# Kernel optimization log

Measured on AMD Instinct MI355X. Metric: run time of the kernel, lower is better.

The kernel has to match this reference:

```python
import jax, jax.numpy as jnp
import numpy as np

B, S, D, H = 4, 2048, 1024, 16
HD = D // H


def setup_inputs() -> dict:
    key = jax.random.key(0)
    ks = jax.random.split(key, 9)
    s = 1.0 / np.sqrt(D)
    return {
        "x": jax.random.normal(ks[0], (B, S, D), dtype=jnp.float32),
        "wq": jax.random.uniform(ks[1], (D, D), jnp.float32, -s, s),
        "bq": jax.random.uniform(ks[2], (D,), jnp.float32, -s, s),
        "wk": jax.random.uniform(ks[3], (D, D), jnp.float32, -s, s),
        "bk": jax.random.uniform(ks[4], (D,), jnp.float32, -s, s),
        "wv": jax.random.uniform(ks[5], (D, D), jnp.float32, -s, s),
        "bv": jax.random.uniform(ks[6], (D,), jnp.float32, -s, s),
        "wo": jax.random.uniform(ks[7], (D, D), jnp.float32, -s, s),
        "bo": jax.random.uniform(ks[8], (D,), jnp.float32, -s, s),
    }


def reference(x, wq, bq, wk, bk, wv, bv, wo, bo):
    b, s, _ = x.shape
    # QKV projections, split into heads: [B, H, S, HD]
    q = (x @ wq + bq).reshape(b, s, H, HD).transpose(0, 2, 1, 3)
    k = (x @ wk + bk).reshape(b, s, H, HD).transpose(0, 2, 1, 3)
    v = (x @ wv + bv).reshape(b, s, H, HD).transpose(0, 2, 1, 3)
    # Full score matrix [B, H, S, S] as the original does
    scores = jnp.einsum("bhqd,bhkd->bhqk", q, k) / jnp.sqrt(jnp.float32(HD))
    attn = jax.nn.softmax(scores, axis=-1)  # dropout is identity in eval mode
    ctx = jnp.einsum("bhqk,bhkd->bhqd", attn, v)
    ctx = ctx.transpose(0, 2, 1, 3).reshape(b, s, D)
    return ctx @ wo + bo
```

## Files before the change

kernel.cpp:

```cpp
#include <hip/hip_runtime.h>
#include <hip/hip_bf16.h>
#include <stdint.h>

#define B_  4
#define S_  2048
#define D_  1024
#define H_  16
#define HD_ 64

using bf16x8 = __attribute__((ext_vector_type(8))) short;
using f32x2  = __attribute__((ext_vector_type(2))) float;
using f32x4  = __attribute__((ext_vector_type(4))) float;
using f32x8  = __attribute__((ext_vector_type(8))) float;
using f32x16 = __attribute__((ext_vector_type(16))) float;
using i32x2  = __attribute__((ext_vector_type(2))) int;
using i32x4  = __attribute__((ext_vector_type(4))) int;

#define QSCALE 0.18033688011112042f

#if __has_builtin(__builtin_amdgcn_exp2f)
#define EXP2F(x) __builtin_amdgcn_exp2f(x)
#else
#define EXP2F(x) exp2f(x)
#endif

__device__ __forceinline__ short f2b(float f) {
  union { __hip_bfloat16 h; short s; } u;
  u.h = __float2bfloat16(f);
  return u.s;
}

__device__ __forceinline__ unsigned cvtpk(float lo, float hi) {
  unsigned r;
  asm("v_cvt_pk_bf16_f32 %0, %1, %2" : "=v"(r) : "v"(lo), "v"(hi));
  return r;
}

__device__ __forceinline__ void g2lds16(const void* g, void* l) {
  __builtin_amdgcn_global_load_lds(
      (const __attribute__((address_space(1))) uint32_t*)(uintptr_t)g,
      (__attribute__((address_space(3))) uint32_t*)(uint32_t)(uintptr_t)l,
      16, 0, 0);
}


__global__ __launch_bounds__(256) void k_cvt_x(
    const float* __restrict__ x, short* __restrict__ xb, int n8,
    const float* __restrict__ bq, const float* __restrict__ bk,
    const float* __restrict__ bv, float* __restrict__ biasqkv) {
  if (blockIdx.x == gridDim.x - 1) {
#pragma unroll
    for (int j = 0; j < 12; ++j) {
      int i = j * 256 + threadIdx.x;
      float v = (i < D_) ? bq[i] * QSCALE : (i < 2 * D_) ? bk[i - D_] : bv[i - 2 * D_];
      biasqkv[i] = v;
    }
    return;
  }
  int i = blockIdx.x * 256 + threadIdx.x;
  if (i >= n8) return;
  const float4* xp = (const float4*)x;
  float4 a = xp[2 * i], b = xp[2 * i + 1];
  bf16x8 o;
  o[0] = f2b(a.x); o[1] = f2b(a.y); o[2] = f2b(a.z); o[3] = f2b(a.w);
  o[4] = f2b(b.x); o[5] = f2b(b.y); o[6] = f2b(b.z); o[7] = f2b(b.w);
  ((bf16x8*)xb)[i] = o;
}

__global__ __launch_bounds__(256) void k_cvt_w(
    const float* __restrict__ wq, const float* __restrict__ wk,
    const float* __restrict__ wv, const float* __restrict__ wo,
    short* __restrict__ wqkvT, short* __restrict__ woT) {
  __shared__ float tile[32][33];
  int wi = blockIdx.z;
  const float* src = wi == 0 ? wq : wi == 1 ? wk : wi == 2 ? wv : wo;
  float scale = (wi == 0) ? QSCALE : 1.0f;
  short* dst = wi < 3 ? wqkvT + (size_t)wi * D_ * D_ : woT;
  int n0 = blockIdx.x * 32, k0 = blockIdx.y * 32;
  int tx = threadIdx.x, ty = threadIdx.y;
#pragma unroll
  for (int j = 0; j < 4; ++j)
    tile[ty + j * 8][tx] = src[(size_t)(k0 + ty + j * 8) * D_ + n0 + tx];
  __syncthreads();
#pragma unroll
  for (int j = 0; j < 4; ++j)
    dst[(size_t)(n0 + ty + j * 8) * D_ + k0 + tx] = f2b(tile[tx][ty + j * 8] * scale);
}


template <int MODE>
__global__ __launch_bounds__(256, 2) void k_gemm(
    const short* __restrict__ A, const short* __restrict__ Bt,
    const float* __restrict__ bias, float* __restrict__ outF,
    short* __restrict__ Qo, short* __restrict__ Ko, short* __restrict__ Vo) {
  constexpr int K = 1024;
  __shared__ short Als[128 * 64];
  __shared__ short Bls[128 * 64];
  const int tid = threadIdx.x;
  const int wave = tid >> 6, lane = tid & 63;
  const int wr = wave >> 1, wc = wave & 1;
  const int l15 = lane & 15, l4 = lane >> 4;
  const int rowBase = blockIdx.x * 128;
  const int colBase = blockIdx.y * 128;

  f32x4 zero4 = {0.f, 0.f, 0.f, 0.f};
  f32x4 acc[4][4];
#pragma unroll
  for (int m = 0; m < 4; ++m)
#pragma unroll
    for (int n = 0; n < 4; ++n) acc[m][n] = zero4;

  for (int kt = 0; kt < K; kt += 64) {
#pragma unroll
    for (int i = 0; i < 4; ++i) {
      int c = i * 256 + tid;
      int r = c >> 3;
      int ko = ((c & 7) * 8) ^ ((r & 7) << 3);
      g2lds16(A + (size_t)(rowBase + r) * K + kt + ko, &Als[(i * 256 + wave * 64) * 8]);
      g2lds16(Bt + (size_t)(colBase + r) * K + kt + ko, &Bls[(i * 256 + wave * 64) * 8]);
    }
    __syncthreads();
#pragma unroll
    for (int kk = 0; kk < 2; ++kk) {
      bf16x8 af[4], bfr[4];
#pragma unroll
      for (int m = 0; m < 4; ++m) {
        int r = wr * 64 + m * 16 + l15;
        af[m] = *(const bf16x8*)&Als[r * 64 + ((kk * 32 + l4 * 8) ^ ((r & 7) << 3))];
      }
#pragma unroll
      for (int n = 0; n < 4; ++n) {
        int r = wc * 64 + n * 16 + l15;
        bfr[n] = *(const bf16x8*)&Bls[r * 64 + ((kk * 32 + l4 * 8) ^ ((r & 7) << 3))];
      }
#pragma unroll
      for (int m = 0; m < 4; ++m)
#pragma unroll
        for (int n = 0; n < 4; ++n)
          acc[m][n] = __builtin_amdgcn_mfma_f32_16x16x32_bf16(af[m], bfr[n], acc[m][n], 0, 0, 0);
    }
    __syncthreads();
  }

#pragma unroll
  for (int n = 0; n < 4; ++n) {
    int n_g = colBase + wc * 64 + n * 16 + l15;
    float bia = bias[n_g];
#pragma unroll
    for (int m = 0; m < 4; ++m) {
#pragma unroll
      for (int r = 0; r < 4; ++r) {
        int m_g = rowBase + wr * 64 + m * 16 + l4 * 4 + r;
        float v = acc[m][n][r] + bia;
        if constexpr (MODE == 0) {
          int p = n_g >> 10, dm = n_g & 1023, h = dm >> 6, hd = dm & 63;
          int b = m_g >> 11, s = m_g & 2047;
          short* dst = p == 0 ? Qo : p == 1 ? Ko : Vo;
          size_t idx;
          if (p == 2) idx = ((size_t)((b * H_ + h) * HD_ + hd)) * S_ + s;
          else        idx = ((size_t)((b * H_ + h) * S_ + s)) * HD_ + hd;
          dst[idx] = f2b(v);
        } else {
          outF[(size_t)m_g * D_ + n_g] = v;
        }
      }
    }
  }
}


__global__ __launch_bounds__(256, 4) void k_attn2(
    const short* __restrict__ Q, const short* __restrict__ K,
    const short* __restrict__ Vt, short* __restrict__ ctx) {
  const int l = blockIdx.x + (blockIdx.y << 4);
  const int c = l & 7, k = l >> 3;
  const int bh = c + ((k & 7) << 3);
  const int q0 = (k >> 3) * 128;
  const int tid = threadIdx.x, wave = tid >> 6, lane = tid & 63;
  const int l31 = lane & 31, hi = lane >> 5;
  const short* Qb = Q + (size_t)bh * S_ * HD_;
  const short* Kb = K + (size_t)bh * S_ * HD_;
  const short* Vb = Vt + (size_t)bh * HD_ * S_;

  __shared__ short Kls[2][64 * 64];
  __shared__ short Vls[2][64 * 64];

  bf16x8 qf[4];
#pragma unroll
  for (int ks = 0; ks < 4; ++ks)
    qf[ks] = *(const bf16x8*)&Qb[(size_t)(q0 + wave * 32 + l31) * HD_ + ks * 16 + hi * 8];

  bf16x8 ones;
#pragma unroll
  for (int i = 0; i < 8; ++i) ones[i] = (short)0x3F80;

  f32x16 ctxa[2], lacc;
#pragma unroll
  for (int i = 0; i < 16; ++i) { ctxa[0][i] = 0.f; ctxa[1][i] = 0.f; lacc[i] = 0.f; }

#define STAGE(kv0, b)                                                          \
  {                                                                            \
    _Pragma("unroll") for (int i = 0; i < 2; ++i) {                            \
      int cc = i * 256 + tid;                                                  \
      int r = cc >> 3;                                                         \
      int off = ((cc & 7) * 8) ^ ((r & 7) << 3);                               \
      g2lds16(Kb + (size_t)((kv0) + r) * HD_ + off,                            \
              &Kls[b][(i * 256 + wave * 64) * 8]);                             \
      g2lds16(Vb + (size_t)r * S_ + (kv0) + off,                               \
              &Vls[b][(i * 256 + wave * 64) * 8]);                             \
    }                                                                          \
  }

  STAGE(0, 0);
  int buf = 0;
#pragma unroll 1
  for (int t = 0; t < S_ / 64; ++t) {
    __syncthreads();
    STAGE((((t + 1) & 31) * 64), (buf ^ 1));

    f32x16 sa[2];
    __builtin_amdgcn_s_setprio(1);
#pragma unroll
    for (int tt = 0; tt < 2; ++tt) {
#pragma unroll
      for (int i = 0; i < 16; ++i) sa[tt][i] = 0.f;
#pragma unroll
      for (int ks = 0; ks < 4; ++ks) {
        int r = tt * 32 + l31;
        bf16x8 kf = *(const bf16x8*)&Kls[buf][r * 64 + ((ks * 16 + hi * 8) ^ ((r & 7) << 3))];
        sa[tt] = __builtin_amdgcn_mfma_f32_32x32x16_bf16(kf, qf[ks], sa[tt], 0, 0, 0);
      }
    }
    __builtin_amdgcn_s_setprio(0);

#pragma unroll
    for (int tt = 0; tt < 2; ++tt)
#pragma unroll
      for (int i = 0; i < 16; ++i) sa[tt][i] = EXP2F(sa[tt][i]);

    __builtin_amdgcn_s_setprio(1);
#pragma unroll
    for (int ks = 0; ks < 4; ++ks) {
      int tt = ks >> 1, s1 = ks & 1;
      unsigned x0 = cvtpk(sa[tt][8 * s1 + 0], sa[tt][8 * s1 + 1]);
      unsigned x1 = cvtpk(sa[tt][8 * s1 + 2], sa[tt][8 * s1 + 3]);
      unsigned y0 = cvtpk(sa[tt][8 * s1 + 4], sa[tt][8 * s1 + 5]);
      unsigned y1 = cvtpk(sa[tt][8 * s1 + 6], sa[tt][8 * s1 + 7]);
      i32x2 r0 = __builtin_amdgcn_permlane32_swap((int)x0, (int)y0, false, false);
      i32x2 r1 = __builtin_amdgcn_permlane32_swap((int)x1, (int)y1, false, false);
      union { i32x4 i; bf16x8 h; } pu;
      pu.i = (i32x4){r0[0], r1[0], r0[1], r1[1]};
      lacc = __builtin_amdgcn_mfma_f32_32x32x16_bf16(ones, pu.h, lacc, 0, 0, 0);
#pragma unroll
      for (int nn = 0; nn < 2; ++nn) {
        int r = nn * 32 + l31;
        bf16x8 vf = *(const bf16x8*)&Vls[buf][r * 64 + ((ks * 16 + hi * 8) ^ ((r & 7) << 3))];
        ctxa[nn] = __builtin_amdgcn_mfma_f32_32x32x16_bf16(vf, pu.h, ctxa[nn], 0, 0, 0);
      }
    }
    __builtin_amdgcn_s_setprio(0);
    buf ^= 1;
  }

  __syncthreads();
  short* Pw = &Kls[0][0] + wave * 2048;
  float inv = 1.0f / lacc[0];
#pragma unroll
  for (int tt = 0; tt < 2; ++tt)
#pragma unroll
    for (int g = 0; g < 4; ++g) {
      unsigned d0 = cvtpk(ctxa[tt][4 * g + 0] * inv, ctxa[tt][4 * g + 1] * inv);
      unsigned d1 = cvtpk(ctxa[tt][4 * g + 2] * inv, ctxa[tt][4 * g + 3] * inv);
      int hd0 = tt * 32 + g * 8 + hi * 4;
      *(i32x2*)((char*)Pw + l31 * 128 + ((hd0 * 2) ^ ((l31 & 7) << 3))) =
          (i32x2){(int)d0, (int)d1};
    }
  __syncthreads();
  const int b = bh >> 4, h = bh & 15;
#pragma unroll
  for (int p = 0; p < 8; ++p) {
    int cc = p * 64 + lane;
    int q = cc >> 4, s8 = cc & 15;
    i32x2 v = *(const i32x2*)((const char*)Pw + q * 128 + ((s8 * 8) ^ ((q & 7) << 3)));
    int row = q0 + wave * 32 + q;
    *(i32x2*)&ctx[((size_t)(b * S_ + row)) * D_ + h * HD_ + s8 * 4] = v;
  }
}


extern "C" void kernel_launch(void* const* d_in, const int* in_sizes, int n_in,
                              void* d_out, int out_size, void* d_ws, size_t ws_size,
                              hipStream_t stream) {
  const float* x  = (const float*)d_in[0];
  const float* wq = (const float*)d_in[1];
  const float* bq = (const float*)d_in[2];
  const float* wk = (const float*)d_in[3];
  const float* bk = (const float*)d_in[4];
  const float* wv = (const float*)d_in[5];
  const float* bv = (const float*)d_in[6];
  const float* wo = (const float*)d_in[7];
  const float* bo = (const float*)d_in[8];
  float* out = (float*)d_out;

  char* ws = (char*)d_ws;
  short* xb    = (short*)(ws);
  short* wqkvT = (short*)(ws + (16 << 20));
  short* woT   = (short*)(ws + (22 << 20));
  float* biasq = (float*)(ws + (24 << 20));
  short* Qb    = (short*)(ws + (25 << 20));
  short* Kb    = (short*)(ws + (41 << 20));
  short* Vb    = (short*)(ws + (57 << 20));

  k_cvt_x<<<dim3(4097), dim3(256), 0, stream>>>(x, xb, (B_ * S_ * D_) / 8,
                                                bq, bk, bv, biasq);
  k_cvt_w<<<dim3(32, 32, 4), dim3(32, 8), 0, stream>>>(wq, wk, wv, wo, wqkvT, woT);

  k_gemm<0><<<dim3(64, 24), dim3(256), 0, stream>>>(xb, wqkvT, biasq,
                                                    (float*)nullptr, Qb, Kb, Vb);
  k_attn2<<<dim3(S_ / 128, B_ * H_), dim3(256), 0, stream>>>(Qb, Kb, Vb, xb );
  k_gemm<1><<<dim3(64, 8), dim3(256), 0, stream>>>(xb, woT, bo, out,
                                                   nullptr, nullptr, nullptr);
}
```

Before: 183.9 us.

## Software-pipeline QK^T one tile ahead of softmax-PV and replace ones-MFMA row sum

Restructures the attention inner loop so the QK^T MFMAs for the next KV tile are issued while the exp and PV work for the current tile runs, with K and V staged on separate schedules in double-buffered LDS. The row-sum MFMA against a ones vector is replaced by a register reduction plus a cross-half lane shuffle. The GEMM launch bound is raised to ask for three blocks per CU. Holding two sets of score accumulators raises register pressure, and the extra occupancy hint may cause spills in the GEMM.

```diff
diff --git a/kernel.cpp b/kernel.cpp
--- a/kernel.cpp
+++ b/kernel.cpp
@@ -89,7 +89,7 @@
 
 
 template <int MODE>
-__global__ __launch_bounds__(256, 2) void k_gemm(
+__global__ __launch_bounds__(256, 3) void k_gemm(
     const short* __restrict__ A, const short* __restrict__ Bt,
     const float* __restrict__ bias, float* __restrict__ outF,
     short* __restrict__ Qo, short* __restrict__ Ko, short* __restrict__ Vo) {
@@ -190,81 +190,107 @@
   for (int ks = 0; ks < 4; ++ks)
     qf[ks] = *(const bf16x8*)&Qb[(size_t)(q0 + wave * 32 + l31) * HD_ + ks * 16 + hi * 8];
 
-  bf16x8 ones;
-#pragma unroll
-  for (int i = 0; i < 8; ++i) ones[i] = (short)0x3F80;
-
-  f32x16 ctxa[2], lacc;
-#pragma unroll
-  for (int i = 0; i < 16; ++i) { ctxa[0][i] = 0.f; ctxa[1][i] = 0.f; lacc[i] = 0.f; }
-
-#define STAGE(kv0, b)                                                          \
+  f32x16 ctxa[2];
+#pragma unroll
+  for (int i = 0; i < 16; ++i) { ctxa[0][i] = 0.f; ctxa[1][i] = 0.f; }
+  float lsum = 0.f;
+
+#define STAGE_K(kvt, b)                                                        \
   {                                                                            \
     _Pragma("unroll") for (int i = 0; i < 2; ++i) {                            \
       int cc = i * 256 + tid;                                                  \
       int r = cc >> 3;                                                         \
       int off = ((cc & 7) * 8) ^ ((r & 7) << 3);                               \
-      g2lds16(Kb + (size_t)((kv0) + r) * HD_ + off,                            \
+      g2lds16(Kb + (size_t)((kvt) * 64 + r) * HD_ + off,                       \
               &Kls[b][(i * 256 + wave * 64) * 8]);                             \
-      g2lds16(Vb + (size_t)r * S_ + (kv0) + off,                               \
+    }                                                                          \
+  }
+#define STAGE_V(kvt, b)                                                        \
+  {                                                                            \
+    _Pragma("unroll") for (int i = 0; i < 2; ++i) {                            \
+      int cc = i * 256 + tid;                                                  \
+      int r = cc >> 3;                                                         \
+      int off = ((cc & 7) * 8) ^ ((r & 7) << 3);                               \
+      g2lds16(Vb + (size_t)r * S_ + (kvt) * 64 + off,                          \
               &Vls[b][(i * 256 + wave * 64) * 8]);                             \
     }                                                                          \
   }
 
-  STAGE(0, 0);
-  int buf = 0;
+#define QKT(s0, s1, b)                                                         \
+  {                                                                            \
+    __builtin_amdgcn_s_setprio(1);                                             \
+    _Pragma("unroll") for (int i = 0; i < 16; ++i) { s0[i] = 0.f; s1[i] = 0.f; } \
+    _Pragma("unroll") for (int ks = 0; ks < 4; ++ks) {                         \
+      int r0 = l31;                                                            \
+      bf16x8 kf0 = *(const bf16x8*)&Kls[b][r0 * 64 +                           \
+                    ((ks * 16 + hi * 8) ^ ((r0 & 7) << 3))];                   \
+      s0 = __builtin_amdgcn_mfma_f32_32x32x16_bf16(kf0, qf[ks], s0, 0, 0, 0);  \
+      int r1 = 32 + l31;                                                       \
+      bf16x8 kf1 = *(const bf16x8*)&Kls[b][r1 * 64 +                           \
+                    ((ks * 16 + hi * 8) ^ ((r1 & 7) << 3))];                   \
+      s1 = __builtin_amdgcn_mfma_f32_32x32x16_bf16(kf1, qf[ks], s1, 0, 0, 0);  \
+    }                                                                          \
+    __builtin_amdgcn_s_setprio(0);                                             \
+  }
+
+#define SMPV(s0, s1, b)                                                        \
+  {                                                                            \
+    _Pragma("unroll") for (int i = 0; i < 16; ++i) {                           \
+      s0[i] = EXP2F(s0[i]); s1[i] = EXP2F(s1[i]);                              \
+    }                                                                          \
+    f32x16 vs = s0 + s1;                                                       \
+    f32x8 a8 = __builtin_shufflevector(vs, vs, 0, 1, 2, 3, 4, 5, 6, 7)         \
+             + __builtin_shufflevector(vs, vs, 8, 9, 10, 11, 12, 13, 14, 15);  \
+    f32x4 a4 = __builtin_shufflevector(a8, a8, 0, 1, 2, 3)                     \
+             + __builtin_shufflevector(a8, a8, 4, 5, 6, 7);                    \
+    f32x2 a2 = __builtin_shufflevector(a4, a4, 0, 1)                           \
+             + __builtin_shufflevector(a4, a4, 2, 3);                          \
+    float rs = a2[0] + a2[1];                                                  \
+    rs += __shfl_xor(rs, 32);                                                  \
+    lsum += rs;                                                                \
+    __builtin_amdgcn_s_setprio(1);                                             \
+    _Pragma("unroll") for (int ks = 0; ks < 4; ++ks) {                         \
+      int s1f = ks & 1;                                                        \
+      float* sp = (ks < 2) ? (float*)&s0 : (float*)&s1;                        \
+      unsigned x0 = cvtpk(sp[8 * s1f + 0], sp[8 * s1f + 1]);                   \
+      unsigned x1 = cvtpk(sp[8 * s1f + 2], sp[8 * s1f + 3]);                   \
+      unsigned y0 = cvtpk(sp[8 * s1f + 4], sp[8 * s1f + 5]);                   \
+      unsigned y1 = cvtpk(sp[8 * s1f + 6], sp[8 * s1f + 7]);                   \
+      i32x2 r0 = __builtin_amdgcn_permlane32_swap((int)x0, (int)y0, false, false); \
+      i32x2 r1 = __builtin_amdgcn_permlane32_swap((int)x1, (int)y1, false, false); \
+      union { i32x4 i; bf16x8 h; } pu;                                         \
+      pu.i = (i32x4){r0[0], r1[0], r0[1], r1[1]};                              \
+      _Pragma("unroll") for (int nn = 0; nn < 2; ++nn) {                       \
+        int r = nn * 32 + l31;                                                 \
+        bf16x8 vf = *(const bf16x8*)&Vls[b][r * 64 +                           \
+                     ((ks * 16 + hi * 8) ^ ((r & 7) << 3))];                   \
+        ctxa[nn] = __builtin_amdgcn_mfma_f32_32x32x16_bf16(vf, pu.h, ctxa[nn], 0, 0, 0); \
+      }                                                                        \
+    }                                                                          \
+    __builtin_amdgcn_s_setprio(0);                                             \
+  }
+
+  f32x16 saA0, saA1, saB0, saB1;
+
+  STAGE_K(0, 0); STAGE_K(1, 1); STAGE_V(0, 0);
+  __syncthreads();
+  QKT(saA0, saA1, 0);
+
 #pragma unroll 1
-  for (int t = 0; t < S_ / 64; ++t) {
+  for (int t = 0; t < 32; t += 2) {
     __syncthreads();
-    STAGE((((t + 1) & 31) * 64), (buf ^ 1));
-
-    f32x16 sa[2];
-    __builtin_amdgcn_s_setprio(1);
-#pragma unroll
-    for (int tt = 0; tt < 2; ++tt) {
-#pragma unroll
-      for (int i = 0; i < 16; ++i) sa[tt][i] = 0.f;
-#pragma unroll
-      for (int ks = 0; ks < 4; ++ks) {
-        int r = tt * 32 + l31;
-        bf16x8 kf = *(const bf16x8*)&Kls[buf][r * 64 + ((ks * 16 + hi * 8) ^ ((r & 7) << 3))];
-        sa[tt] = __builtin_amdgcn_mfma_f32_32x32x16_bf16(kf, qf[ks], sa[tt], 0, 0, 0);
-      }
-    }
-    __builtin_amdgcn_s_setprio(0);
-
-#pragma unroll
-    for (int tt = 0; tt < 2; ++tt)
-#pragma unroll
-      for (int i = 0; i < 16; ++i) sa[tt][i] = EXP2F(sa[tt][i]);
-
-    __builtin_amdgcn_s_setprio(1);
-#pragma unroll
-    for (int ks = 0; ks < 4; ++ks) {
-      int tt = ks >> 1, s1 = ks & 1;
-      unsigned x0 = cvtpk(sa[tt][8 * s1 + 0], sa[tt][8 * s1 + 1]);
-      unsigned x1 = cvtpk(sa[tt][8 * s1 + 2], sa[tt][8 * s1 + 3]);
-      unsigned y0 = cvtpk(sa[tt][8 * s1 + 4], sa[tt][8 * s1 + 5]);
-      unsigned y1 = cvtpk(sa[tt][8 * s1 + 6], sa[tt][8 * s1 + 7]);
-      i32x2 r0 = __builtin_amdgcn_permlane32_swap((int)x0, (int)y0, false, false);
-      i32x2 r1 = __builtin_amdgcn_permlane32_swap((int)x1, (int)y1, false, false);
-      union { i32x4 i; bf16x8 h; } pu;
-      pu.i = (i32x4){r0[0], r1[0], r0[1], r1[1]};
-      lacc = __builtin_amdgcn_mfma_f32_32x32x16_bf16(ones, pu.h, lacc, 0, 0, 0);
-#pragma unroll
-      for (int nn = 0; nn < 2; ++nn) {
-        int r = nn * 32 + l31;
-        bf16x8 vf = *(const bf16x8*)&Vls[buf][r * 64 + ((ks * 16 + hi * 8) ^ ((r & 7) << 3))];
-        ctxa[nn] = __builtin_amdgcn_mfma_f32_32x32x16_bf16(vf, pu.h, ctxa[nn], 0, 0, 0);
-      }
-    }
-    __builtin_amdgcn_s_setprio(0);
-    buf ^= 1;
+    STAGE_K((t + 2) & 31, 0); STAGE_V((t + 1) & 31, 1);
+    QKT(saB0, saB1, 1);
+    SMPV(saA0, saA1, 0);
+    __syncthreads();
+    STAGE_K((t + 3) & 31, 1); STAGE_V((t + 2) & 31, 0);
+    QKT(saA0, saA1, 0);
+    SMPV(saB0, saB1, 1);
   }
 
   __syncthreads();
   short* Pw = &Kls[0][0] + wave * 2048;
-  float inv = 1.0f / lacc[0];
+  float inv = 1.0f / lsum;
 #pragma unroll
   for (int tt = 0; tt < 2; ++tt)
 #pragma unroll
```

After: 269.8 us. 1.47x slower.
